# Optimization experiments

Hardware: AMD Instinct MI355X
Metric: run time of the kernel (lower is better)

The kernel has to match this reference:

```python
import jax, jax.numpy as jnp
import numpy as np

DIM = 256
N_EMBED = 4096


def setup_inputs() -> dict:
    key = jax.random.key(0)
    k1, k2 = jax.random.split(key)
    input = jax.random.normal(k1, (8, 64, 64, DIM), dtype=jnp.float32)
    embed = jax.random.normal(k2, (DIM, N_EMBED), dtype=jnp.float32)
    return {"input": input, "embed": embed}


def reference(input, embed):
    # flatten: [N, dim]
    flatten = input.reshape(-1, DIM)
    # squared-euclidean distance to each code: [N, n_embed]
    dist = (
        jnp.sum(flatten * flatten, axis=1, keepdims=True)
        - 2.0 * flatten @ embed
        + jnp.sum(embed * embed, axis=0, keepdims=True)
    )
    embed_ind_flat = jnp.argmax(-dist, axis=1)  # nearest code per vector
    embed_ind = embed_ind_flat.reshape(input.shape[:-1])
    # gather codes: embed is [dim, n_embed], codebook rows are embed.T
    quantize = jnp.take(embed.T, embed_ind, axis=0)  # [B, m, n, dim]
    # commitment loss (quantize detached)
    diff = jnp.mean((jax.lax.stop_gradient(quantize) - input) ** 2)
    # straight-through estimator
    quantize = input + jax.lax.stop_gradient(quantize - input)
    return (quantize, diff, embed_ind)
```

## Files before the change

kernel.cpp:

```cpp
#include <hip/hip_runtime.h>
#include <hip/hip_bf16.h>


#define M_ROWS 32768
#define K_DIM 256
#define N_CODES 4096

typedef __attribute__((ext_vector_type(8))) short short8v;
typedef __attribute__((ext_vector_type(4))) float f32x4;

__device__ inline unsigned long long packKey(float d, int idx) {
    unsigned u = __float_as_uint(d);
    u = (u & 0x80000000u) ? ~u : (u | 0x80000000u);
    return ((unsigned long long)u << 32) | (unsigned)idx;
}
__device__ inline float unpackDist(unsigned long long k) {
    unsigned u = (unsigned)(k >> 32);
    u = (u & 0x80000000u) ? (u & 0x7FFFFFFFu) : ~u;
    return __uint_as_float(u);
}
__device__ inline unsigned short f2bf(float x) {
    __hip_bfloat16 h = __float2bfloat16(x);
    return *reinterpret_cast<unsigned short*>(&h);
}
__device__ inline unsigned long long u64min(unsigned long long a, unsigned long long b) {
    return a < b ? a : b;
}
__device__ inline unsigned long long u64max(unsigned long long a, unsigned long long b) {
    return a > b ? a : b;
}

__device__ inline float serial_dot(const float4* __restrict__ fr,
                                   const float4* __restrict__ er) {
    float ex = 0.f;
    for (int k4 = 0; k4 < 64; ++k4) {
        float4 a = fr[k4], b = er[k4];
        ex = fmaf(a.x, b.x, ex); ex = fmaf(a.y, b.y, ex);
        ex = fmaf(a.z, b.z, ex); ex = fmaf(a.w, b.w, ex);
    }
    return ex;
}

__global__ void transpose_kernel(const float* __restrict__ E,
                                 float* __restrict__ Et,
                                 unsigned short* __restrict__ Ethi) {
    __shared__ float tile[64][65];
    const int kb = blockIdx.x & 3;
    const int jb = blockIdx.x >> 2;
    const int t = threadIdx.x;
#pragma unroll
    for (int it = 0; it < 16; ++it) {
        int linear = it * 256 + t;
        int kk = linear >> 6, jj = linear & 63;
        tile[kk][jj] = E[(size_t)(kb * 64 + kk) * N_CODES + jb * 64 + jj];
    }
    __syncthreads();
#pragma unroll
    for (int it = 0; it < 16; ++it) {
        int linear = it * 256 + t;
        int jj = linear >> 6, kk = linear & 63;
        float v = tile[kk][jj];
        size_t o = (size_t)(jb * 64 + jj) * K_DIM + kb * 64 + kk;
        Et[o] = v;
        Ethi[o] = f2bf(v);
    }
}

__global__ void nrm_et_kernel(const float* __restrict__ Et,
                              float* __restrict__ nrm,
                              float* __restrict__ maxnrm) {
    const int l = threadIdx.x & 63;
    const int j = blockIdx.x * 4 + (threadIdx.x >> 6);
    float4 v = *(const float4*)&Et[(size_t)j * K_DIM + l * 4];
    float s = v.x * v.x;
    s = fmaf(v.y, v.y, s); s = fmaf(v.z, v.z, s); s = fmaf(v.w, v.w, s);
#pragma unroll
    for (int sh = 32; sh >= 1; sh >>= 1) s += __shfl_xor(s, sh, 64);
    if (l == 0) {
        nrm[j] = s;
        atomicMax((int*)maxnrm, __float_as_int(s));
    }
}

__global__ __launch_bounds__(512) void gemm_top2_kernel(
    const float* __restrict__ F,
    const unsigned short* __restrict__ Ethi,
    const float* __restrict__ nrm,
    unsigned long long* __restrict__ keys2)
{
    __shared__ unsigned short sA[256 * 64];
    __shared__ unsigned short sB[256 * 64];
    const int tid = threadIdx.x;
    const int l = tid & 63;
    const int wid = tid >> 6;
    const int tile = (blockIdx.x & 7) * 256 + (blockIdx.x >> 3);
    const int by = tile >> 4, bx = tile & 15;
    const int bm0 = by * 256, bn0 = bx * 256;
    const int wm = wid >> 1, wn = wid & 1;

    f32x4 acc[4][8];
#pragma unroll
    for (int mi = 0; mi < 4; ++mi)
#pragma unroll
        for (int ni = 0; ni < 8; ++ni) acc[mi][ni] = (f32x4){0.f, 0.f, 0.f, 0.f};

    const float* aSrc = F + (size_t)(bm0 + wid * 32 + (l >> 1)) * K_DIM + (l & 1) * 32;
    const int arow = wid * 32 + (l >> 1);

#pragma unroll
    for (int kt = 0; kt < 4; ++kt) {
        float4 areg[8];
#pragma unroll
        for (int i = 0; i < 8; ++i)
            areg[i] = *(const float4*)(aSrc + kt * 64 + i * 4);

        if (kt > 0) __syncthreads();

#pragma unroll
        for (int j = 0; j < 4; ++j) {
            short8v hv;
            hv[0] = (short)f2bf(areg[2 * j].x);     hv[1] = (short)f2bf(areg[2 * j].y);
            hv[2] = (short)f2bf(areg[2 * j].z);     hv[3] = (short)f2bf(areg[2 * j].w);
            hv[4] = (short)f2bf(areg[2 * j + 1].x); hv[5] = (short)f2bf(areg[2 * j + 1].y);
            hv[6] = (short)f2bf(areg[2 * j + 1].z); hv[7] = (short)f2bf(areg[2 * j + 1].w);
            int c = (l & 1) * 4 + j, phys = c ^ (arow & 7);
            *(short8v*)&sA[arow * 64 + phys * 8] = hv;
        }
#pragma unroll
        for (int i = 0; i < 4; ++i) {
            int q = wid * 4 + i;
            const unsigned short* src = Ethi +
                (size_t)(bn0 + q * 8 + (l >> 3)) * K_DIM + kt * 64 +
                ((l & 7) ^ (l >> 3)) * 8;
            __builtin_amdgcn_global_load_lds(
                (const __attribute__((address_space(1))) unsigned int*)src,
                (__attribute__((address_space(3))) unsigned int*)&sB[q * 512],
                16, 0, 0);
        }
        __syncthreads();

#pragma unroll
        for (int s = 0; s < 2; ++s) {
            const int ch = s * 4 + (l >> 4);
            short8v af[4], bfv[8];
#pragma unroll
            for (int mi = 0; mi < 4; ++mi) {
                int r = wm * 64 + mi * 16 + (l & 15);
                af[mi] = *(const short8v*)&sA[r * 64 + (ch ^ (r & 7)) * 8];
            }
#pragma unroll
            for (int ni = 0; ni < 8; ++ni) {
                int c = wn * 128 + ni * 16 + (l & 15);
                bfv[ni] = *(const short8v*)&sB[c * 64 + (ch ^ (c & 7)) * 8];
            }
#pragma unroll
            for (int mi = 0; mi < 4; ++mi)
#pragma unroll
                for (int ni = 0; ni < 8; ++ni)
                    acc[mi][ni] = __builtin_amdgcn_mfma_f32_16x16x32_bf16(
                        af[mi], bfv[ni], acc[mi][ni], 0, 0, 0);
        }
    }

    float nv[8];
#pragma unroll
    for (int ni = 0; ni < 8; ++ni)
        nv[ni] = nrm[bn0 + wn * 128 + ni * 16 + (l & 15)];

#pragma unroll
    for (int mi = 0; mi < 4; ++mi)
#pragma unroll
        for (int rr = 0; rr < 4; ++rr) {
            unsigned long long k1 = ~0ull, k2 = ~0ull;
#pragma unroll
            for (int ni = 0; ni < 8; ++ni) {
                float d = fmaf(-2.f, acc[mi][ni][rr], nv[ni]);
                unsigned long long kk =
                    packKey(d, bn0 + wn * 128 + ni * 16 + (l & 15));
                if (kk < k1) { k2 = k1; k1 = kk; }
                else if (kk < k2) { k2 = kk; }
            }
#pragma unroll
            for (int st = 1; st < 16; st <<= 1) {
                unsigned long long o1 = __shfl_xor(k1, st, 64);
                unsigned long long o2 = __shfl_xor(k2, st, 64);
                unsigned long long hi = u64max(k1, o1);
                k1 = u64min(k1, o1);
                k2 = u64min(u64min(k2, o2), hi);
            }
            if ((l & 15) == 0) {
                int row = bm0 + wm * 64 + mi * 16 + (l >> 4) * 4 + rr;
                int g = bx * 2 + wn;
                keys2[(size_t)row * 64 + g * 2]     = k1;
                keys2[(size_t)row * 64 + g * 2 + 1] = k2;
            }
        }
}

__global__ __launch_bounds__(256) void rescore_kernel(
    const float* __restrict__ F,
    const float* __restrict__ Et,
    const float* __restrict__ nrm,
    const float* __restrict__ maxnrm,
    const unsigned long long* __restrict__ keys2,
    float* __restrict__ q_out,
    float* __restrict__ diff_out,
    float* __restrict__ ind_out)
{
    __shared__ float wpart[4];
    const int l = threadIdx.x & 63;
    const int wid = threadIdx.x >> 6;
    const float mxn = maxnrm[0];
    float ldiff = 0.f;
    const int rbase = (blockIdx.x * 4 + wid) * 8;

    for (int rr = 0; rr < 8; ++rr) {
        const int row = rbase + rr;
        const unsigned long long* slots = keys2 + (size_t)row * 64;
        const float4* fr = (const float4*)&F[(size_t)row * K_DIM];

        unsigned long long k = slots[l];
        float dk = unpackDist(k);
        float m = dk;
#pragma unroll
        for (int s = 1; s < 64; s <<= 1) m = fminf(m, __shfl_xor(m, s, 64));
        float4 x4 = fr[l];
        float nx = x4.x * x4.x;
        nx = fmaf(x4.y, x4.y, nx); nx = fmaf(x4.z, x4.z, nx); nx = fmaf(x4.w, x4.w, nx);
#pragma unroll
        for (int s = 1; s < 64; s <<= 1) nx += __shfl_xor(nx, s, 64);
        const float thr = m + 0.05f * sqrtf(nx * mxn) + 0.25f;

        const unsigned long long cm = __ballot(dk <= thr);
        unsigned long long bestk = ~0ull;

        {
            unsigned long long t = cm;
            for (int i = 0; i < l && t; ++i) t &= t - 1;
            if (t) {
                int b = __ffsll(t) - 1;
                int c = (int)(slots[b] & 0xffffffffull);
                float ex = serial_dot(fr, (const float4*)&Et[(size_t)c * K_DIM]);
                bestk = packKey(fmaf(-2.f, ex, nrm[c]), c);
            }
        }
        unsigned long long fg = cm & 0xAAAAAAAAAAAAAAAAull;
        while (fg) {
            int b = __ffsll(fg) - 1;
            fg &= fg - 1;
            int g = b >> 1;
#pragma unroll
            for (int h = 0; h < 2; ++h) {
                int c = g * 128 + h * 64 + l;
                float ex = serial_dot(fr, (const float4*)&Et[(size_t)c * K_DIM]);
                bestk = u64min(bestk, packKey(fmaf(-2.f, ex, nrm[c]), c));
            }
        }
#pragma unroll
        for (int s = 1; s < 64; s <<= 1)
            bestk = u64min(bestk, __shfl_xor(bestk, s, 64));

        const unsigned cstar = (unsigned)(bestk & 0xffffffffull);
        float4 e4 = *(const float4*)&Et[(size_t)cstar * K_DIM + l * 4];
        float d0 = e4.x - x4.x, d1 = e4.y - x4.y, d2 = e4.z - x4.z, d3 = e4.w - x4.w;
        float4 o = {x4.x + d0, x4.y + d1, x4.z + d2, x4.w + d3};
        *(float4*)&q_out[(size_t)row * K_DIM + l * 4] = o;
        ldiff = fmaf(d0, d0, ldiff); ldiff = fmaf(d1, d1, ldiff);
        ldiff = fmaf(d2, d2, ldiff); ldiff = fmaf(d3, d3, ldiff);
        if (l == 0) ind_out[row] = (float)cstar;
    }
#pragma unroll
    for (int s = 1; s < 64; s <<= 1) ldiff += __shfl_xor(ldiff, s, 64);
    if (l == 0) wpart[wid] = ldiff;
    __syncthreads();
    if (threadIdx.x == 0) {
        float t = 0.f;
#pragma unroll
        for (int i = 0; i < 4; ++i) t += wpart[i];
        atomicAdd(diff_out, t * (1.0f / ((float)M_ROWS * (float)K_DIM)));
    }
}

__global__ void norms_kernel(const float* __restrict__ E, float* __restrict__ norms) {
    int j = blockIdx.x * blockDim.x + threadIdx.x;
    if (j >= N_CODES) return;
    float s = 0.f;
    for (int d = 0; d < K_DIM; ++d) {
        float v = E[(size_t)d * N_CODES + j];
        s = fmaf(v, v, s);
    }
    norms[j] = s;
}

__global__ __launch_bounds__(256, 2) void gemm_argmin_kernel(
    const float* __restrict__ F, const float* __restrict__ E,
    const float* __restrict__ norms, unsigned long long* __restrict__ keys) {
    __shared__ float As[32][132];
    __shared__ float Bs[32][132];
    const int bx = blockIdx.x & 31, by = blockIdx.x >> 5;
    const int bm0 = by * 128, bn0 = bx * 128;
    const int tid = threadIdx.x;
    const int tx = tid & 15, ty = tid >> 4;
    float acc[8][8];
#pragma unroll
    for (int i = 0; i < 8; ++i)
#pragma unroll
        for (int j = 0; j < 8; ++j) acc[i][j] = 0.f;
    for (int kc = 0; kc < K_DIM; kc += 32) {
        float4 a_reg[4], b_reg[4];
#pragma unroll
        for (int i = 0; i < 4; ++i) {
            int idx = tid + i * 256;
            int m = idx >> 3, k4 = idx & 7;
            a_reg[i] = *(const float4*)&F[(size_t)(bm0 + m) * K_DIM + kc + k4 * 4];
            int kk = idx >> 5, n4 = idx & 31;
            b_reg[i] = *(const float4*)&E[(size_t)(kc + kk) * N_CODES + bn0 + n4 * 4];
        }
        __syncthreads();
#pragma unroll
        for (int i = 0; i < 4; ++i) {
            int idx = tid + i * 256;
            int m = idx >> 3, k4 = idx & 7;
            As[k4 * 4 + 0][m] = a_reg[i].x; As[k4 * 4 + 1][m] = a_reg[i].y;
            As[k4 * 4 + 2][m] = a_reg[i].z; As[k4 * 4 + 3][m] = a_reg[i].w;
            int kk = idx >> 5, n4 = idx & 31;
            *(float4*)&Bs[kk][n4 * 4] = b_reg[i];
        }
        __syncthreads();
#pragma unroll
        for (int k = 0; k < 32; ++k) {
            float a[8], b[8];
            *(float4*)&a[0] = *(const float4*)&As[k][ty * 8];
            *(float4*)&a[4] = *(const float4*)&As[k][ty * 8 + 4];
            *(float4*)&b[0] = *(const float4*)&Bs[k][tx * 8];
            *(float4*)&b[4] = *(const float4*)&Bs[k][tx * 8 + 4];
#pragma unroll
            for (int i = 0; i < 8; ++i)
#pragma unroll
                for (int j = 0; j < 8; ++j) acc[i][j] = fmaf(a[i], b[j], acc[i][j]);
        }
    }
    float nrm8[8];
#pragma unroll
    for (int j = 0; j < 8; ++j) nrm8[j] = norms[bn0 + tx * 8 + j];
#pragma unroll
    for (int i = 0; i < 8; ++i) {
        float best = INFINITY; int bestj = 0;
#pragma unroll
        for (int j = 0; j < 8; ++j) {
            float d = fmaf(-2.f, acc[i][j], nrm8[j]);
            if (d < best) { best = d; bestj = bn0 + tx * 8 + j; }
        }
        unsigned long long key = packKey(best, bestj);
#pragma unroll
        for (int s = 1; s < 16; s <<= 1) {
            unsigned long long o = __shfl_xor(key, s, 64);
            if (o < key) key = o;
        }
        if (tx == 0) atomicMin(&keys[bm0 + ty * 8 + i], key);
    }
}

__global__ void gather_legacy_kernel(
    const float* __restrict__ F, const float* __restrict__ E,
    const unsigned long long* __restrict__ keys,
    float* __restrict__ q_out, float* __restrict__ diff_out,
    float* __restrict__ ind_out) {
    const int lane = threadIdx.x & 63;
    const int wave = (blockIdx.x * (blockDim.x >> 6)) + (threadIdx.x >> 6);
    const int nwaves = gridDim.x * (blockDim.x >> 6);
    float dsum = 0.f;
    for (int row = wave; row < M_ROWS; row += nwaves) {
        int ind = (int)(keys[row] & 0xFFFFFFFFull);
        if (lane == 0) ind_out[row] = (float)ind;
#pragma unroll
        for (int t = 0; t < 4; ++t) {
            int d = lane + t * 64;
            float x = F[(size_t)row * K_DIM + d];
            float q = E[(size_t)d * N_CODES + ind];
            float delta = q - x;
            q_out[(size_t)row * K_DIM + d] = x + delta;
            dsum = fmaf(delta, delta, dsum);
        }
    }
#pragma unroll
    for (int s = 32; s >= 1; s >>= 1) dsum += __shfl_xor(dsum, s, 64);
    if (lane == 0)
        atomicAdd(diff_out, dsum * (1.0f / ((float)M_ROWS * (float)K_DIM)));
}

extern "C" void kernel_launch(void* const* d_in, const int* in_sizes, int n_in,
                              void* d_out, int out_size, void* d_ws, size_t ws_size,
                              hipStream_t stream) {
    const float* F = (const float*)d_in[0];
    const float* E = (const float*)d_in[1];

    float* q_out = (float*)d_out;
    float* diff_out = q_out + (size_t)M_ROWS * K_DIM;
    float* ind_out = diff_out + 1;

    const size_t off_nrm  = 0;
    const size_t off_mx   = 16384;
    const size_t off_Et   = 32768;
    const size_t off_Ethi = off_Et + (size_t)N_CODES * K_DIM * 4;
    const size_t off_k2   = off_Ethi + (size_t)N_CODES * K_DIM * 2;
    const size_t NEED     = off_k2 + (size_t)M_ROWS * 64 * 8;

    if (ws_size >= NEED) {
        float* nrm = (float*)((char*)d_ws + off_nrm);
        float* maxnrm = (float*)((char*)d_ws + off_mx);
        float* Et = (float*)((char*)d_ws + off_Et);
        unsigned short* Ethi = (unsigned short*)((char*)d_ws + off_Ethi);
        unsigned long long* keys2 = (unsigned long long*)((char*)d_ws + off_k2);

        hipMemsetAsync(maxnrm, 0, 4, stream);
        hipMemsetAsync(diff_out, 0, 4, stream);

        transpose_kernel<<<256, 256, 0, stream>>>(E, Et, Ethi);
        nrm_et_kernel<<<1024, 256, 0, stream>>>(Et, nrm, maxnrm);
        gemm_top2_kernel<<<2048, 512, 0, stream>>>(F, Ethi, nrm, keys2);
        rescore_kernel<<<1024, 256, 0, stream>>>(F, Et, nrm, maxnrm, keys2,
                                                 q_out, diff_out, ind_out);
    } else {
        float* norms = (float*)d_ws;
        unsigned long long* keys = (unsigned long long*)((char*)d_ws + 16384);
        hipMemsetAsync(keys, 0xFF, (size_t)M_ROWS * 8, stream);
        hipMemsetAsync(diff_out, 0, 4, stream);
        norms_kernel<<<N_CODES / 256, 256, 0, stream>>>(E, norms);
        gemm_argmin_kernel<<<(M_ROWS / 128) * (N_CODES / 128), 256, 0, stream>>>(F, E, norms, keys);
        gather_legacy_kernel<<<1024, 256, 0, stream>>>(F, E, keys, q_out, diff_out, ind_out);
    }
}
```

Baseline: 825.5 us.

## Stage rescore candidate rows in LDS with coalesced loads, one row per wave

The rescore kernel now gives each wave one row instead of eight and launches eight times as many blocks. Candidate codebook rows are loaded cooperatively with coalesced float4 loads into padded shared memory, eight at a time. Each of eight lanes then runs a serial dot product from LDS, replacing per-lane strided global reads of whole codebook rows. This trades uncoalesced global traffic for LDS staging and low lane utilisation (only 8 of 64 lanes compute). The fallback full-group path now processes 128 codes in 16 serial batches rather than 2 fully parallel passes.

```diff
diff --git a/kernel.cpp b/kernel.cpp
--- a/kernel.cpp
+++ b/kernel.cpp
@@ -30,11 +30,12 @@
     return a > b ? a : b;
 }
 
-__device__ inline float serial_dot(const float4* __restrict__ fr,
-                                   const float4* __restrict__ er) {
+__device__ inline float serial_dot_lds(const float* __restrict__ fp,
+                                       const float* __restrict__ cp) {
     float ex = 0.f;
     for (int k4 = 0; k4 < 64; ++k4) {
-        float4 a = fr[k4], b = er[k4];
+        float4 a = *(const float4*)&fp[k4 * 4];
+        float4 b = *(const float4*)&cp[k4 * 4];
         ex = fmaf(a.x, b.x, ex); ex = fmaf(a.y, b.y, ex);
         ex = fmaf(a.z, b.z, ex); ex = fmaf(a.w, b.w, ex);
     }
@@ -197,6 +198,7 @@
         }
 }
 
+#define CSTRIDE 260
 __global__ __launch_bounds__(256) void rescore_kernel(
     const float* __restrict__ F,
     const float* __restrict__ Et,
@@ -207,68 +209,94 @@
     float* __restrict__ diff_out,
     float* __restrict__ ind_out)
 {
+    __shared__ float sf[4][256];
+    __shared__ float sc[4][8][CSTRIDE];
     __shared__ float wpart[4];
     const int l = threadIdx.x & 63;
     const int wid = threadIdx.x >> 6;
     const float mxn = maxnrm[0];
+    const int row = blockIdx.x * 4 + wid;
+
+    const unsigned long long* slots = keys2 + (size_t)row * 64;
+
+    unsigned long long k = slots[l];
+    float4 x4 = *(const float4*)&F[(size_t)row * K_DIM + l * 4];
+    float dk = unpackDist(k);
+    const int myc = (int)(k & 0xffffffffull);
+
+    *(float4*)&sf[wid][l * 4] = x4;
+
+    float m = dk;
+#pragma unroll
+    for (int s = 1; s < 64; s <<= 1) m = fminf(m, __shfl_xor(m, s, 64));
+    float nx = x4.x * x4.x;
+    nx = fmaf(x4.y, x4.y, nx); nx = fmaf(x4.z, x4.z, nx); nx = fmaf(x4.w, x4.w, nx);
+#pragma unroll
+    for (int s = 1; s < 64; s <<= 1) nx += __shfl_xor(nx, s, 64);
+    const float thr = m + 0.05f * sqrtf(nx * mxn) + 0.25f;
+
+    const unsigned long long cm = __ballot(dk <= thr);
+    unsigned long long bestk = ~0ull;
+    const float* fp = &sf[wid][0];
+
+    unsigned long long mrem = cm;
+    while (mrem) {
+        int nb = 0;
+        int mycand = -1;
+#pragma unroll
+        for (int i = 0; i < 8; ++i) {
+            if (mrem) {
+                int b = __ffsll(mrem) - 1;
+                mrem &= mrem - 1;
+                int c = __shfl(myc, b, 64);
+                *(float4*)&sc[wid][i][l * 4] =
+                    *(const float4*)&Et[(size_t)c * K_DIM + l * 4];
+                if (l == i) mycand = c;
+                ++nb;
+            }
+        }
+        if (l < nb) {
+            const float* cp = &sc[wid][0][0] + (size_t)l * CSTRIDE;
+            float ex = serial_dot_lds(fp, cp);
+            bestk = u64min(bestk, packKey(fmaf(-2.f, ex, nrm[mycand]), mycand));
+        }
+    }
+
+    unsigned long long fg = cm & 0xAAAAAAAAAAAAAAAAull;
+    while (fg) {
+        int b = __ffsll(fg) - 1;
+        fg &= fg - 1;
+        int g = b >> 1;
+        for (int t = 0; t < 16; ++t) {
+#pragma unroll
+            for (int i = 0; i < 8; ++i) {
+                int c = g * 128 + t * 8 + i;
+                *(float4*)&sc[wid][i][l * 4] =
+                    *(const float4*)&Et[(size_t)c * K_DIM + l * 4];
+            }
+            if (l < 8) {
+                int c = g * 128 + t * 8 + l;
+                const float* cp = &sc[wid][0][0] + (size_t)l * CSTRIDE;
+                float ex = serial_dot_lds(fp, cp);
+                bestk = u64min(bestk, packKey(fmaf(-2.f, ex, nrm[c]), c));
+            }
+        }
+    }
+
+#pragma unroll
+    for (int s = 1; s < 64; s <<= 1)
+        bestk = u64min(bestk, __shfl_xor(bestk, s, 64));
+
+    const unsigned cstar = (unsigned)(bestk & 0xffffffffull);
+    float4 e4 = *(const float4*)&Et[(size_t)cstar * K_DIM + l * 4];
+    float d0 = e4.x - x4.x, d1 = e4.y - x4.y, d2 = e4.z - x4.z, d3 = e4.w - x4.w;
+    float4 o = {x4.x + d0, x4.y + d1, x4.z + d2, x4.w + d3};
+    *(float4*)&q_out[(size_t)row * K_DIM + l * 4] = o;
     float ldiff = 0.f;
-    const int rbase = (blockIdx.x * 4 + wid) * 8;
-
-    for (int rr = 0; rr < 8; ++rr) {
-        const int row = rbase + rr;
-        const unsigned long long* slots = keys2 + (size_t)row * 64;
-        const float4* fr = (const float4*)&F[(size_t)row * K_DIM];
-
-        unsigned long long k = slots[l];
-        float dk = unpackDist(k);
-        float m = dk;
-#pragma unroll
-        for (int s = 1; s < 64; s <<= 1) m = fminf(m, __shfl_xor(m, s, 64));
-        float4 x4 = fr[l];
-        float nx = x4.x * x4.x;
-        nx = fmaf(x4.y, x4.y, nx); nx = fmaf(x4.z, x4.z, nx); nx = fmaf(x4.w, x4.w, nx);
-#pragma unroll
-        for (int s = 1; s < 64; s <<= 1) nx += __shfl_xor(nx, s, 64);
-        const float thr = m + 0.05f * sqrtf(nx * mxn) + 0.25f;
-
-        const unsigned long long cm = __ballot(dk <= thr);
-        unsigned long long bestk = ~0ull;
-
-        {
-            unsigned long long t = cm;
-            for (int i = 0; i < l && t; ++i) t &= t - 1;
-            if (t) {
-                int b = __ffsll(t) - 1;
-                int c = (int)(slots[b] & 0xffffffffull);
-                float ex = serial_dot(fr, (const float4*)&Et[(size_t)c * K_DIM]);
-                bestk = packKey(fmaf(-2.f, ex, nrm[c]), c);
-            }
-        }
-        unsigned long long fg = cm & 0xAAAAAAAAAAAAAAAAull;
-        while (fg) {
-            int b = __ffsll(fg) - 1;
-            fg &= fg - 1;
-            int g = b >> 1;
-#pragma unroll
-            for (int h = 0; h < 2; ++h) {
-                int c = g * 128 + h * 64 + l;
-                float ex = serial_dot(fr, (const float4*)&Et[(size_t)c * K_DIM]);
-                bestk = u64min(bestk, packKey(fmaf(-2.f, ex, nrm[c]), c));
-            }
-        }
-#pragma unroll
-        for (int s = 1; s < 64; s <<= 1)
-            bestk = u64min(bestk, __shfl_xor(bestk, s, 64));
-
-        const unsigned cstar = (unsigned)(bestk & 0xffffffffull);
-        float4 e4 = *(const float4*)&Et[(size_t)cstar * K_DIM + l * 4];
-        float d0 = e4.x - x4.x, d1 = e4.y - x4.y, d2 = e4.z - x4.z, d3 = e4.w - x4.w;
-        float4 o = {x4.x + d0, x4.y + d1, x4.z + d2, x4.w + d3};
-        *(float4*)&q_out[(size_t)row * K_DIM + l * 4] = o;
-        ldiff = fmaf(d0, d0, ldiff); ldiff = fmaf(d1, d1, ldiff);
-        ldiff = fmaf(d2, d2, ldiff); ldiff = fmaf(d3, d3, ldiff);
-        if (l == 0) ind_out[row] = (float)cstar;
-    }
+    ldiff = fmaf(d0, d0, ldiff); ldiff = fmaf(d1, d1, ldiff);
+    ldiff = fmaf(d2, d2, ldiff); ldiff = fmaf(d3, d3, ldiff);
+    if (l == 0) ind_out[row] = (float)cstar;
+
 #pragma unroll
     for (int s = 1; s < 64; s <<= 1) ldiff += __shfl_xor(ldiff, s, 64);
     if (l == 0) wpart[wid] = ldiff;
@@ -419,7 +447,7 @@
         transpose_kernel<<<256, 256, 0, stream>>>(E, Et, Ethi);
         nrm_et_kernel<<<1024, 256, 0, stream>>>(Et, nrm, maxnrm);
         gemm_top2_kernel<<<2048, 512, 0, stream>>>(F, Ethi, nrm, keys2);
-        rescore_kernel<<<1024, 256, 0, stream>>>(F, Et, nrm, maxnrm, keys2,
+        rescore_kernel<<<8192, 256, 0, stream>>>(F, Et, nrm, maxnrm, keys2,
                                                  q_out, diff_out, ind_out);
     } else {
         float* norms = (float*)d_ws;
```

Measured after the change: 933.8 us. +13.1%, slower.
